# Kernel optimization log

Hardware: AMD Instinct MI355X
Metric: run time of the kernel (lower is better)

## Reference

```python
import jax, jax.numpy as jnp
import numpy as np

N_HEAD = 16


def setup_inputs() -> dict:
    B, T, C, H = 64, 128, 2048, N_HEAD
    hd = C // H
    key = jax.random.key(0)
    ks = jax.random.split(key, 5)
    x = jax.random.normal(ks[0], (B, T, C), dtype=jnp.float32)
    wq = jax.random.normal(ks[1], (C, C), dtype=jnp.float32) * 0.02
    wk = jax.random.normal(ks[2], (C, C), dtype=jnp.float32) * 0.02
    wv = jax.random.normal(ks[3], (C, C), dtype=jnp.float32) * 0.02
    wo = jax.random.normal(ks[4], (C, C), dtype=jnp.float32) * 0.02
    # RoPE frequencies: freqs_cis = exp(i * pos * theta_j), theta_j = 10000^(-2j/hd)
    pos = jnp.arange(T, dtype=jnp.float32)
    inv_freq = 1.0 / (10000.0 ** (jnp.arange(0, hd, 2, dtype=jnp.float32) / hd))  # [hd/2]
    ang = pos[:, None] * inv_freq[None, :]  # [T, hd/2]
    return {
        "x": x,
        "freqs_cos": jnp.cos(ang),
        "freqs_sin": jnp.sin(ang),
        "wq": wq, "wk": wk, "wv": wv, "wo": wo,
    }


def _apply_rope(t, cos, sin):
    # t: [B,T,H,hd]; complex multiply on interleaved (even, odd) pairs
    B, T, H, hd = t.shape
    tr = t.reshape(B, T, H, hd // 2, 2)
    te, to = tr[..., 0], tr[..., 1]
    c = cos[None, :, None, :]  # [1,T,1,hd/2]
    s = sin[None, :, None, :]
    oe = te * c - to * s
    oo = te * s + to * c
    return jnp.stack([oe, oo], axis=-1).reshape(B, T, H, hd)


def reference(x, freqs_cos, freqs_sin, wq, wk, wv, wo):
    B, T, C = x.shape
    H = N_HEAD
    hd = C // H
    q = (x @ wq.T).reshape(B, T, H, hd)
    k = (x @ wk.T).reshape(B, T, H, hd)
    v = (x @ wv.T).reshape(B, T, H, hd)
    q = _apply_rope(q, freqs_cos, freqs_sin)
    k = _apply_rope(k, freqs_cos, freqs_sin)
    # scores: [B,H,T,S]
    scores = jnp.einsum("bthd,bshd->bhts", q, k) / (hd ** 0.5)
    causal = jnp.tril(jnp.ones((T, T), dtype=bool))
    scores = jnp.where(causal[None, None], scores, jnp.float32(-jnp.inf))
    probs = jax.nn.softmax(scores, axis=-1)  # dropout is identity in eval
    out = jnp.einsum("bhts,bshd->bthd", probs, v).reshape(B, T, C)
    return out @ wo.T
```

## Files before the change

kernel.cpp:

```cpp
#include <hip/hip_runtime.h>
#include <cstdint>


typedef unsigned short ushort;
typedef __bf16 bf16x8 __attribute__((ext_vector_type(8)));
typedef float floatx4 __attribute__((ext_vector_type(4)));

__device__ __forceinline__ ushort f2bf(float f) {
  union { float f; uint32_t u; } v; v.f = f;
  uint32_t r = v.u + 0x7FFFu + ((v.u >> 16) & 1u);
  return (ushort)(r >> 16);
}
__device__ __forceinline__ float bf2f(ushort h) {
  union { uint32_t u; float f; } v; v.u = ((uint32_t)h) << 16;
  return v.f;
}

__device__ __forceinline__ void load_lds16(const void* g, void* l) {
  __builtin_amdgcn_global_load_lds(
      (__attribute__((address_space(1))) void*)(uintptr_t)g,
      (__attribute__((address_space(3))) void*)(uint32_t)(uintptr_t)l,
      16, 0, 0);
}

__device__ __forceinline__ void store_out(ushort* C, size_t i, float v) { C[i] = f2bf(v); }
__device__ __forceinline__ void store_out(float* C, size_t i, float v) { C[i] = v; }

__device__ __forceinline__ void phase_mid() {
  __builtin_amdgcn_s_barrier();
  asm volatile("s_waitcnt lgkmcnt(0)" ::: "memory");
  __builtin_amdgcn_sched_barrier(0);
}
__device__ __forceinline__ void phase_end() {
  __builtin_amdgcn_s_barrier();
  __builtin_amdgcn_sched_barrier(0);
}

template <typename OutT>
__device__ __forceinline__ void gemm256_body(const ushort* __restrict__ A,
                                             const ushort* __restrict__ B,
                                             OutT* __restrict__ C,
                                             int M, int N, int K) {
  (void)M;
  __shared__ __align__(16) ushort As[2][256 * 64];
  __shared__ __align__(16) ushort Bs[2][256 * 64];
  const int tid = threadIdx.x;
  const int wave = tid >> 6, lane = tid & 63;
  const int quad = lane >> 4, colv = lane & 15;
  const int wm = wave & 1, wn = wave >> 1;
  const int m0 = blockIdx.x * 256, n0 = blockIdx.y * 256;

  const int a_base = (wm * 128 + colv) * 64;
  const int b_base = (wn * 64 + colv) * 64;
  const int kg0 = ((quad) ^ (colv & 7)) << 3;
  const int kg1 = ((quad | 4) ^ (colv & 7)) << 3;

  const int srow = tid >> 3;
  const int scol = ((tid & 7) ^ (srow & 7)) << 3;
  const ushort* Ag = A + (size_t)(m0 + srow) * K + scol;
  const ushort* Bg = B + (size_t)(n0 + srow) * K + scol;
  const int ldsw = wave * 512;

  floatx4 acc[8][4] = {};
  bf16x8 af[4][2], bfr[4][2];

#define STAGE(Gb, T, half, kt)                                             \
  {                                                                        \
    const ushort* g_ = (Gb) + (size_t)((half) * 128) * K + (kt) * 64;      \
    load_lds16(g_, &(T)[(half) * 8192 + ldsw]);                            \
    load_lds16(g_ + (size_t)64 * K, &(T)[(half) * 8192 + 4096 + ldsw]);    \
  }

#define READ_B_ALL(bi)                                                     \
  _Pragma("unroll") for (int nf = 0; nf < 4; ++nf) {                       \
    bfr[nf][0] = *(const bf16x8*)&Bs[bi][b_base + nf * 1024 + kg0];        \
    bfr[nf][1] = *(const bf16x8*)&Bs[bi][b_base + nf * 1024 + kg1];        \
  }

#define READ_A(bi, off)                                                    \
  _Pragma("unroll") for (int mf = 0; mf < 4; ++mf) {                       \
    af[mf][0] = *(const bf16x8*)&As[bi][a_base + (off) + mf * 1024 + kg0]; \
    af[mf][1] = *(const bf16x8*)&As[bi][a_base + (off) + mf * 1024 + kg1]; \
  }

#define MFMA16(ks, mo)                                                     \
  __builtin_amdgcn_s_setprio(1);                                           \
  _Pragma("unroll") for (int mf = 0; mf < 4; ++mf)                         \
  _Pragma("unroll") for (int nf = 0; nf < 4; ++nf)                         \
    acc[(mo) + mf][nf] = __builtin_amdgcn_mfma_f32_16x16x32_bf16(          \
        af[mf][(ks)], bfr[nf][(ks)], acc[(mo) + mf][nf], 0, 0, 0);         \
  __builtin_amdgcn_s_setprio(0);

  STAGE(Bg, Bs[0], 0, 0)
  STAGE(Bg, Bs[0], 1, 0)
  STAGE(Ag, As[0], 0, 0)
  STAGE(Ag, As[0], 1, 0)
  STAGE(Bg, Bs[1], 0, 1)
  STAGE(Bg, Bs[1], 1, 1)
  STAGE(Ag, As[1], 0, 1)
  asm volatile("s_waitcnt vmcnt(6)" ::: "memory");
  __builtin_amdgcn_s_barrier();
  __builtin_amdgcn_sched_barrier(0);

  const int NT = K >> 6;
#pragma unroll 1
  for (int it = 0; it < (NT >> 1); ++it) {
    const int s0 = (2 * it + 2 < NT) ? 2 * it + 2 : NT - 1;
    const int s1 = (2 * it + 3 < NT) ? 2 * it + 3 : NT - 1;

    READ_B_ALL(0)
    READ_A(0, 0)
    STAGE(Ag, As[1], 1, 2 * it + 1)
    phase_mid();
    MFMA16(0, 0)
    phase_end();
    STAGE(Bg, Bs[0], 0, s0)
    phase_mid();
    MFMA16(1, 0)
    phase_end();
    READ_A(0, 4096)
    STAGE(Bg, Bs[0], 1, s0)
    phase_mid();
    MFMA16(0, 4)
    phase_end();
    STAGE(Ag, As[0], 0, s0)
    asm volatile("s_waitcnt vmcnt(6)" ::: "memory");
    phase_mid();
    MFMA16(1, 4)
    phase_end();
    READ_B_ALL(1)
    READ_A(1, 0)
    STAGE(Ag, As[0], 1, s0)
    phase_mid();
    MFMA16(0, 0)
    phase_end();
    STAGE(Bg, Bs[1], 0, s1)
    phase_mid();
    MFMA16(1, 0)
    phase_end();
    READ_A(1, 4096)
    STAGE(Bg, Bs[1], 1, s1)
    phase_mid();
    MFMA16(0, 4)
    phase_end();
    STAGE(Ag, As[1], 0, s1)
    asm volatile("s_waitcnt vmcnt(6)" ::: "memory");
    phase_mid();
    MFMA16(1, 4)
    phase_end();
  }
  asm volatile("s_waitcnt vmcnt(0)" ::: "memory");

#pragma unroll
  for (int mf = 0; mf < 8; ++mf)
#pragma unroll
    for (int nf = 0; nf < 4; ++nf)
#pragma unroll
      for (int r = 0; r < 4; ++r) {
        int m = m0 + wm * 128 + mf * 16 + quad * 4 + r;
        int n = n0 + wn * 64 + nf * 16 + colv;
        store_out(C, (size_t)m * N + n, acc[mf][nf][r]);
      }
#undef STAGE
#undef READ_B_ALL
#undef READ_A
#undef MFMA16
}

__global__ __launch_bounds__(512) void gemm_qkv(
    const ushort* __restrict__ A, const ushort* __restrict__ Wq,
    const ushort* __restrict__ Wk, const ushort* __restrict__ Wv,
    ushort* __restrict__ Q, ushort* __restrict__ Kb, ushort* __restrict__ V) {
  const ushort* B = (blockIdx.z == 0) ? Wq : (blockIdx.z == 1) ? Wk : Wv;
  ushort* C = (blockIdx.z == 0) ? Q : (blockIdx.z == 1) ? Kb : V;
  gemm256_body<ushort>(A, B, C, 8192, 2048, 2048);
}

__global__ __launch_bounds__(512) void gemm_out_k(
    const ushort* __restrict__ A, const ushort* __restrict__ B,
    float* __restrict__ C) {
  gemm256_body<float>(A, B, C, 8192, 2048, 2048);
}

#define NX 4194304u
#define NW 1048576u
__global__ void cvt_all(const float* __restrict__ x, const float* __restrict__ wq,
                        const float* __restrict__ wk, const float* __restrict__ wv,
                        const float* __restrict__ wo,
                        ushort* __restrict__ xb, ushort* __restrict__ wqb,
                        ushort* __restrict__ wkb, ushort* __restrict__ wvb,
                        ushort* __restrict__ wob) {
  uint32_t i = blockIdx.x * 256u + threadIdx.x;
  const float* src;
  ushort* dst;
  uint32_t off;
  if (i < NX) {
    src = x; dst = xb; off = i;
  } else {
    uint32_t i2 = i - NX;
    uint32_t r = i2 >> 20;
    off = i2 & (NW - 1u);
    src = (r == 0) ? wq : (r == 1) ? wk : (r == 2) ? wv : wo;
    dst = (r == 0) ? wqb : (r == 1) ? wkb : (r == 2) ? wvb : wob;
  }
  float4 v = ((const float4*)src)[off];
  ushort4 o;
  o.x = f2bf(v.x); o.y = f2bf(v.y); o.z = f2bf(v.z); o.w = f2bf(v.w);
  ((ushort4*)dst)[off] = o;
}

__global__ __launch_bounds__(256) void attn_kernel(
    const ushort* __restrict__ Q, const ushort* __restrict__ K,
    const ushort* __restrict__ V, const float* __restrict__ Cf,
    const float* __restrict__ Sf, ushort* __restrict__ O) {
  __shared__ __align__(16) ushort Qs[128 * 128];
  __shared__ __align__(16) ushort KVs[128 * 128];
  const int b = blockIdx.x >> 4, h = blockIdx.x & 15;
  const int tid = threadIdx.x, wave = tid >> 6, lane = tid & 63;
  const int quad = lane >> 4, colv = lane & 15;
  const size_t gbase = (size_t)b * 262144 + (size_t)h * 128;

#pragma unroll
  for (int sgi = 0; sgi < 8; ++sgi) {
    int seg = tid + sgi * 256;
    int t = seg >> 4, g = seg & 15;
    uint4 qv = *(const uint4*)(Q + gbase + (size_t)t * 2048 + g * 8);
    uint4 kv = *(const uint4*)(K + gbase + (size_t)t * 2048 + g * 8);
    float4 cf = *(const float4*)(Cf + t * 64 + g * 4);
    float4 sf = *(const float4*)(Sf + t * 64 + g * 4);
    uint32_t* qw = (uint32_t*)&qv;
    uint32_t* kw = (uint32_t*)&kv;
#pragma unroll
    for (int j = 0; j < 4; ++j) {
      float c = (&cf.x)[j], s = (&sf.x)[j];
      uint32_t w = qw[j];
      float e = bf2f((ushort)(w & 0xFFFF)), o = bf2f((ushort)(w >> 16));
      qw[j] = (uint32_t)f2bf(e * c - o * s) | ((uint32_t)f2bf(e * s + o * c) << 16);
      w = kw[j];
      e = bf2f((ushort)(w & 0xFFFF)); o = bf2f((ushort)(w >> 16));
      kw[j] = (uint32_t)f2bf(e * c - o * s) | ((uint32_t)f2bf(e * s + o * c) << 16);
    }
    int so = t * 128 + ((g ^ (t & 15)) << 3);
    *(uint4*)&Qs[so] = qv;
    *(uint4*)&KVs[so] = kv;
  }
  __syncthreads();

  floatx4 accs[2][8] = {};
#pragma unroll
  for (int kc = 0; kc < 4; ++kc) {
    bf16x8 af[2], bfr[8];
#pragma unroll
    for (int i = 0; i < 2; ++i) {
      int r = wave * 32 + i * 16 + colv;
      af[i] = *(const bf16x8*)&Qs[r * 128 + ((((kc << 2) | quad) ^ (r & 15)) << 3)];
    }
#pragma unroll
    for (int j = 0; j < 8; ++j) {
      int r = j * 16 + colv;
      bfr[j] = *(const bf16x8*)&KVs[r * 128 + ((((kc << 2) | quad) ^ (r & 15)) << 3)];
    }
#pragma unroll
    for (int i = 0; i < 2; ++i)
#pragma unroll
      for (int j = 0; j < 8; ++j)
        accs[i][j] = __builtin_amdgcn_mfma_f32_16x16x32_bf16(af[i], bfr[j], accs[i][j], 0, 0, 0);
  }

  const float scale = 0.08838834764831845f;
#pragma unroll
  for (int i = 0; i < 2; ++i)
#pragma unroll
    for (int r = 0; r < 4; ++r) {
      int t = wave * 32 + i * 16 + quad * 4 + r;
      float mx = -1e30f;
#pragma unroll
      for (int j = 0; j < 8; ++j) {
        int s = j * 16 + colv;
        float v = accs[i][j][r] * scale;
        v = (s <= t) ? v : -1e30f;
        accs[i][j][r] = v;
        mx = fmaxf(mx, v);
      }
#pragma unroll
      for (int off = 1; off < 16; off <<= 1) mx = fmaxf(mx, __shfl_xor(mx, off, 64));
      float l = 0.f;
#pragma unroll
      for (int j = 0; j < 8; ++j) {
        float p = __expf(accs[i][j][r] - mx);
        accs[i][j][r] = p;
        l += p;
      }
#pragma unroll
      for (int off = 1; off < 16; off <<= 1) l += __shfl_xor(l, off, 64);
      float inv = 1.0f / l;
#pragma unroll
      for (int j = 0; j < 8; ++j) {
        int s = j * 16 + colv;
        Qs[t * 128 + ((((s >> 3) ^ (t & 15)) << 3) | (s & 7))] = f2bf(accs[i][j][r] * inv);
      }
    }
  __syncthreads();

#pragma unroll
  for (int sgi = 0; sgi < 8; ++sgi) {
    int seg = tid + sgi * 256;
    int t = seg >> 4;
    int dg = (seg & 15) << 3;
    uint4 vv = *(const uint4*)(V + gbase + (size_t)t * 2048 + dg);
    const ushort* vp = (const ushort*)&vv;
#pragma unroll
    for (int jj = 0; jj < 8; ++jj) {
      int d = dg + jj;
      KVs[d * 128 + ((((t >> 3) ^ (d & 15)) << 3) | (t & 7))] = vp[jj];
    }
  }
  __syncthreads();

  floatx4 acco[2][8] = {};
#pragma unroll
  for (int kc = 0; kc < 4; ++kc) {
    bf16x8 af[2], bfr[8];
#pragma unroll
    for (int i = 0; i < 2; ++i) {
      int r = wave * 32 + i * 16 + colv;
      af[i] = *(const bf16x8*)&Qs[r * 128 + ((((kc << 2) | quad) ^ (r & 15)) << 3)];
    }
#pragma unroll
    for (int j = 0; j < 8; ++j) {
      int r = j * 16 + colv;
      bfr[j] = *(const bf16x8*)&KVs[r * 128 + ((((kc << 2) | quad) ^ (r & 15)) << 3)];
    }
#pragma unroll
    for (int i = 0; i < 2; ++i)
#pragma unroll
      for (int j = 0; j < 8; ++j)
        acco[i][j] = __builtin_amdgcn_mfma_f32_16x16x32_bf16(af[i], bfr[j], acco[i][j], 0, 0, 0);
  }

#pragma unroll
  for (int i = 0; i < 2; ++i)
#pragma unroll
    for (int j = 0; j < 8; ++j)
#pragma unroll
      for (int r = 0; r < 4; ++r) {
        int t = wave * 32 + i * 16 + quad * 4 + r;
        int d = j * 16 + colv;
        O[gbase + (size_t)t * 2048 + d] = f2bf(acco[i][j][r]);
      }
}

extern "C" void kernel_launch(void* const* d_in, const int* in_sizes, int n_in,
                              void* d_out, int out_size, void* d_ws, size_t ws_size,
                              hipStream_t stream) {
  const float* x    = (const float*)d_in[0];
  const float* fcos = (const float*)d_in[1];
  const float* fsin = (const float*)d_in[2];
  const float* wq   = (const float*)d_in[3];
  const float* wk   = (const float*)d_in[4];
  const float* wv   = (const float*)d_in[5];
  const float* wo   = (const float*)d_in[6];
  float* out = (float*)d_out;

  const size_t CC = 2048ull * 2048ull;
  const size_t MC = 8192ull * 2048ull;
  ushort* wob = (ushort*)d_ws;
  ushort* xb  = wob + CC;
  ushort* wqb = xb + MC;
  ushort* wkb = wqb + CC;
  ushort* wvb = wkb + CC;
  ushort* Qb  = wvb + CC;
  ushort* Kb  = Qb + MC;
  ushort* Vb  = Kb + MC;

  unsigned cvt_blocks = (unsigned)((MC + 4 * CC) / 4 / 256);
  cvt_all<<<dim3(cvt_blocks), 256, 0, stream>>>(x, wq, wk, wv, wo, xb, wqb, wkb, wvb, wob);

  gemm_qkv<<<dim3(32, 8, 3), 512, 0, stream>>>(xb, wqb, wkb, wvb, Qb, Kb, Vb);
  attn_kernel<<<dim3(1024), 256, 0, stream>>>(Qb, Kb, Vb, fcos, fsin, xb);
  gemm_out_k<<<dim3(32, 8), 512, 0, stream>>>(xb, wob, out);
}
```

Baseline: 448.2 us.

## Prefetch V early, stage attention output through LDS, grid-stride conversion kernel

The conversion kernel becomes a grid-stride loop over 2048 blocks, each thread handling 16 float4s, instead of one element per thread. In attention, V is loaded into registers alongside Q and K and transposed into LDS right after the QK MFMAs, removing a separate global-load phase and one barrier. The output is staged through a padded LDS tile so it can be written as coalesced 16-byte stores instead of scattered 2-byte stores. It also adds s_setprio around the MFMA loops and launch_bounds(256,2), at the cost of more register pressure from holding V for the whole score phase.

```diff
diff --git a/kernel.cpp b/kernel.cpp
--- a/kernel.cpp
+++ b/kernel.cpp
@@ -182,50 +182,57 @@
   gemm256_body<float>(A, B, C, 8192, 2048, 2048);
 }
 
-#define NX 4194304u
-#define NW 1048576u
-__global__ void cvt_all(const float* __restrict__ x, const float* __restrict__ wq,
-                        const float* __restrict__ wk, const float* __restrict__ wv,
-                        const float* __restrict__ wo,
-                        ushort* __restrict__ xb, ushort* __restrict__ wqb,
-                        ushort* __restrict__ wkb, ushort* __restrict__ wvb,
-                        ushort* __restrict__ wob) {
-  uint32_t i = blockIdx.x * 256u + threadIdx.x;
-  const float* src;
-  ushort* dst;
-  uint32_t off;
-  if (i < NX) {
-    src = x; dst = xb; off = i;
-  } else {
-    uint32_t i2 = i - NX;
-    uint32_t r = i2 >> 20;
-    off = i2 & (NW - 1u);
-    src = (r == 0) ? wq : (r == 1) ? wk : (r == 2) ? wv : wo;
-    dst = (r == 0) ? wqb : (r == 1) ? wkb : (r == 2) ? wvb : wob;
-  }
-  float4 v = ((const float4*)src)[off];
-  ushort4 o;
-  o.x = f2bf(v.x); o.y = f2bf(v.y); o.z = f2bf(v.z); o.w = f2bf(v.w);
-  ((ushort4*)dst)[off] = o;
-}
-
-__global__ __launch_bounds__(256) void attn_kernel(
+#define NX4  4194304u
+#define NW4  1048576u
+__global__ __launch_bounds__(256) void cvt_all(
+    const float* __restrict__ x, const float* __restrict__ wq,
+    const float* __restrict__ wk, const float* __restrict__ wv,
+    const float* __restrict__ wo,
+    ushort* __restrict__ xb, ushort* __restrict__ wqb,
+    ushort* __restrict__ wkb, ushort* __restrict__ wvb,
+    ushort* __restrict__ wob) {
+  const uint32_t i0 = blockIdx.x * 256u + threadIdx.x;
+#pragma unroll
+  for (uint32_t u = 0; u < 16u; ++u) {
+    uint32_t i = i0 + u * 524288u;
+    const float* src;
+    ushort* dst;
+    uint32_t off;
+    if (i < NX4) {
+      src = x; dst = xb; off = i;
+    } else {
+      uint32_t i2 = i - NX4;
+      uint32_t r = i2 >> 20;
+      off = i2 & (NW4 - 1u);
+      src = (r == 0) ? wq : (r == 1) ? wk : (r == 2) ? wv : wo;
+      dst = (r == 0) ? wqb : (r == 1) ? wkb : (r == 2) ? wvb : wob;
+    }
+    float4 v = ((const float4*)src)[off];
+    ushort4 o;
+    o.x = f2bf(v.x); o.y = f2bf(v.y); o.z = f2bf(v.z); o.w = f2bf(v.w);
+    ((ushort4*)dst)[off] = o;
+  }
+}
+
+__global__ __launch_bounds__(256, 2) void attn_kernel(
     const ushort* __restrict__ Q, const ushort* __restrict__ K,
     const ushort* __restrict__ V, const float* __restrict__ Cf,
     const float* __restrict__ Sf, ushort* __restrict__ O) {
-  __shared__ __align__(16) ushort Qs[128 * 128];
+  __shared__ __align__(16) ushort Qs[128 * 136];
   __shared__ __align__(16) ushort KVs[128 * 128];
   const int b = blockIdx.x >> 4, h = blockIdx.x & 15;
   const int tid = threadIdx.x, wave = tid >> 6, lane = tid & 63;
   const int quad = lane >> 4, colv = lane & 15;
   const size_t gbase = (size_t)b * 262144 + (size_t)h * 128;
 
+  uint4 vreg[8];
 #pragma unroll
   for (int sgi = 0; sgi < 8; ++sgi) {
     int seg = tid + sgi * 256;
     int t = seg >> 4, g = seg & 15;
     uint4 qv = *(const uint4*)(Q + gbase + (size_t)t * 2048 + g * 8);
     uint4 kv = *(const uint4*)(K + gbase + (size_t)t * 2048 + g * 8);
+    vreg[sgi] = *(const uint4*)(V + gbase + (size_t)t * 2048 + g * 8);
     float4 cf = *(const float4*)(Cf + t * 64 + g * 4);
     float4 sf = *(const float4*)(Sf + t * 64 + g * 4);
     uint32_t* qw = (uint32_t*)&qv;
@@ -260,11 +267,27 @@
       int r = j * 16 + colv;
       bfr[j] = *(const bf16x8*)&KVs[r * 128 + ((((kc << 2) | quad) ^ (r & 15)) << 3)];
     }
+    __builtin_amdgcn_s_setprio(1);
 #pragma unroll
     for (int i = 0; i < 2; ++i)
 #pragma unroll
       for (int j = 0; j < 8; ++j)
         accs[i][j] = __builtin_amdgcn_mfma_f32_16x16x32_bf16(af[i], bfr[j], accs[i][j], 0, 0, 0);
+    __builtin_amdgcn_s_setprio(0);
+  }
+  __syncthreads();
+
+#pragma unroll
+  for (int sgi = 0; sgi < 8; ++sgi) {
+    int seg = tid + sgi * 256;
+    int t = seg >> 4;
+    int dg = (seg & 15) << 3;
+    const ushort* vp = (const ushort*)&vreg[sgi];
+#pragma unroll
+    for (int jj = 0; jj < 8; ++jj) {
+      int d = dg + jj;
+      KVs[d * 128 + ((((t >> 3) ^ (d & 15)) << 3) | (t & 7))] = vp[jj];
+    }
   }
 
   const float scale = 0.08838834764831845f;
@@ -302,21 +325,6 @@
     }
   __syncthreads();
 
-#pragma unroll
-  for (int sgi = 0; sgi < 8; ++sgi) {
-    int seg = tid + sgi * 256;
-    int t = seg >> 4;
-    int dg = (seg & 15) << 3;
-    uint4 vv = *(const uint4*)(V + gbase + (size_t)t * 2048 + dg);
-    const ushort* vp = (const ushort*)&vv;
-#pragma unroll
-    for (int jj = 0; jj < 8; ++jj) {
-      int d = dg + jj;
-      KVs[d * 128 + ((((t >> 3) ^ (d & 15)) << 3) | (t & 7))] = vp[jj];
-    }
-  }
-  __syncthreads();
-
   floatx4 acco[2][8] = {};
 #pragma unroll
   for (int kc = 0; kc < 4; ++kc) {
@@ -331,12 +339,15 @@
       int r = j * 16 + colv;
       bfr[j] = *(const bf16x8*)&KVs[r * 128 + ((((kc << 2) | quad) ^ (r & 15)) << 3)];
     }
+    __builtin_amdgcn_s_setprio(1);
 #pragma unroll
     for (int i = 0; i < 2; ++i)
 #pragma unroll
       for (int j = 0; j < 8; ++j)
         acco[i][j] = __builtin_amdgcn_mfma_f32_16x16x32_bf16(af[i], bfr[j], acco[i][j], 0, 0, 0);
-  }
+    __builtin_amdgcn_s_setprio(0);
+  }
+  __syncthreads();
 
 #pragma unroll
   for (int i = 0; i < 2; ++i)
@@ -346,8 +357,14 @@
       for (int r = 0; r < 4; ++r) {
         int t = wave * 32 + i * 16 + quad * 4 + r;
         int d = j * 16 + colv;
-        O[gbase + (size_t)t * 2048 + d] = f2bf(acco[i][j][r]);
-      }
+        Qs[t * 136 + d] = f2bf(acco[i][j][r]);
+      }
+#pragma unroll
+  for (int g = 0; g < 8; ++g) {
+    int row = wave * 32 + g * 4 + quad;
+    uint4 ov = *(const uint4*)&Qs[row * 136 + colv * 8];
+    *(uint4*)(O + gbase + (size_t)row * 2048 + colv * 8) = ov;
+  }
 }
 
 extern "C" void kernel_launch(void* const* d_in, const int* in_sizes, int n_in,
@@ -373,8 +390,7 @@
   ushort* Kb  = Qb + MC;
   ushort* Vb  = Kb + MC;
 
-  unsigned cvt_blocks = (unsigned)((MC + 4 * CC) / 4 / 256);
-  cvt_all<<<dim3(cvt_blocks), 256, 0, stream>>>(x, wq, wk, wv, wo, xb, wqb, wkb, wvb, wob);
+  cvt_all<<<dim3(2048), 256, 0, stream>>>(x, wq, wk, wv, wo, xb, wqb, wkb, wvb, wob);
 
   gemm_qkv<<<dim3(32, 8, 3), 512, 0, stream>>>(xb, wqb, wkb, wvb, Qb, Kb, Vb);
   attn_kernel<<<dim3(1024), 256, 0, stream>>>(Qb, Kb, Vb, fcos, fsin, xb);
```

After: 448.4 us. No clear change (+0.0%).
